# Kernel tuning notes

Measured on AMD Instinct MI355X. Metric: run time of the kernel, lower is better.

The kernel has to match this reference:

```python
import jax, jax.numpy as jnp
import numpy as np

N, D1, D2, B = 8, 2048, 1024, 512
D = D1 * D2
MAXBW = 3
NUM_PART = 5          # num_possible_partitions
TEMP = 0.01           # TEMPERATURE used in df_lt
DENOS = (3.0, 5.0, 17.0)  # 2^2-1, 2^2+1, 2^4+1


def ste_floor(x):
    # straight-through floor: forward floor, backward identity
    return x + jax.lax.stop_gradient(jnp.floor(x) - x)


def segmented_mean(piece, scheme, msp):
    """Replicates the inner python scan over sorted rows.
    piece:  (N, D) sorted residual errors
    scheme: (N-1, D) rounded split decisions (0/1), per column
    msp:    (N-1, D) soft split probabilities (grad factors), per column
    Returns (N, D): each row gets grad_ * (segment mean) of its segment.
    """
    n = piece.shape[0]
    buf = jnp.zeros_like(piece[0])
    cnt = jnp.zeros_like(piece[0])
    g = jnp.ones_like(piece[0])
    reset = jnp.zeros(piece.shape[1], dtype=bool)
    vlist, blist = [], []
    for i in range(n):
        buf = jnp.where(reset, piece[i], buf + piece[i])
        cnt = jnp.where(reset, 1.0, cnt + 1.0)
        g = jnp.where(reset, 1.0, g)
        if i == n - 1:
            vlist.append(g * (buf / cnt))
            blist.append(jnp.ones_like(reset))
        else:
            b = scheme[i] > 0.5
            vlist.append(jnp.where(b, g * msp[i], 0.0) * (buf / cnt))
            blist.append(b)
            g = jnp.where(b, g, g * (1.0 - msp[i]))
            reset = b
    # broadcast each segment-end value back to all rows of its segment
    out = vlist[-1]
    outs = [out]
    for i in range(n - 2, -1, -1):
        out = jnp.where(blist[i], vlist[i], out)
        outs.append(out)
    return jnp.stack(outs[::-1], axis=0)


def residual_quant(U, vsum, s, thr):
    """One residual quantization level (the update_partition=True branch)."""
    res = U - vsum                                   # (N, D)
    idx_maps = jnp.argsort(res, axis=0)              # torch.sort ascending, dim=0
    sorted_err = jnp.take_along_axis(res, idx_maps, axis=0)
    delta = sorted_err[1:] - sorted_err[:-1]         # (N-1, D), >= 0
    delta = delta / jnp.max(delta)
    msp = jax.nn.sigmoid((delta - thr) / TEMP)       # mean_split_point (N-1, D)
    rs = jnp.round(msp)                              # round_split, 0/1

    nm1 = N - 1
    P = 2 ** nm1  # all possible split-column patterns (torch.unique over dim=1)
    weights = (2 ** jnp.arange(nm1 - 1, -1, -1)).astype(jnp.int32)  # row 0 = MSB (lexicographic)
    code = jnp.sum(rs.astype(jnp.int32) * weights[:, None], axis=0)  # (D,)
    counts = jnp.zeros((P,), jnp.int32).at[code].add(1)
    present = counts > 0
    # torch.unique sorts patterns lexicographically -> rank = #present codes below
    rank_of_code = jnp.cumsum(present.astype(jnp.int32)) - present.astype(jnp.int32)
    order = jnp.argsort(-counts)                     # codes by count descending
    top_codes = order[:NUM_PART]
    top_ranks = rank_of_code[top_codes]              # s_indices[:NUM_PART]
    # binary patterns for every possible code
    patterns = ((jnp.arange(P)[:, None] >> jnp.arange(nm1 - 1, -1, -1)[None, :]) & 1).astype(jnp.float32)  # (P, N-1)
    inter = patterns @ patterns[top_codes].T         # (P, NUM_PART)
    sel = jnp.argmax(inter, axis=1)
    reassigned = top_ranks[sel]                      # (P,)
    is_top = jnp.any(rank_of_code[:, None] == top_ranks[None, :], axis=1)
    final_rank = jnp.where(is_top, rank_of_code, reassigned)  # (P,)
    c_rank = final_rank[code]                        # clustered_indices, (D,)

    # NOTE: original indexes round_split / mean_split_point columns BY the
    # unique-cluster index value s_idx (a quirk of the source); replicate it.
    scheme_used = rs[:, c_rank]                      # (N-1, D)
    msp_used = msp[:, c_rank]                        # (N-1, D)

    inner = segmented_mean(sorted_err, scheme_used, msp_used)  # (N, D)
    # einsum('cb,cba->ab', inner, one_hot(idx_maps)) == unsort along dim 0
    inv = jnp.argsort(idx_maps, axis=0)
    grouped = jnp.take_along_axis(inner, inv, axis=0)
    return s * ste_floor(grouped / s)


def setup_inputs():
    key = jax.random.key(0)
    k1, k2 = jax.random.split(key)
    x = jax.random.normal(k1, (B, N, D1), dtype=jnp.float32)
    # kaiming_normal_ on (N, D): std = sqrt(2 / fan_in), fan_in = D
    U = jax.random.normal(k2, (N, D), dtype=jnp.float32) * np.float32(np.sqrt(2.0 / D))
    thres_mean = jnp.full((D2,), -1.3, dtype=jnp.float32)
    return {"x": x, "U": U, "thres_mean": thres_mean}


def reference(x, U, thres_mean):
    beta = jnp.max(U)
    alpha = jnp.min(U)
    s = (beta - alpha) / DENOS[0]
    vsum = s * ste_floor(U / s)                      # base quantization level
    thr = jax.nn.sigmoid(jnp.repeat(thres_mean, D1))  # thres_mean.repeat_interleave(D1)
    for deno in DENOS[1:MAXBW]:
        s = s / deno
        vsum = vsum + residual_quant(U, vsum, s, thr)
    w = vsum.reshape(N, D1, D2)
    return jnp.einsum('bnd,ndl->bnl', x, w)
```

## Files before the change

kernel.cpp:

```cpp
#include <hip/hip_runtime.h>
#include <hip/hip_bf16.h>
#include <math.h>

#define NROW 8
#define DT   2097152
#define DD1  2048
#define DD2  1024
#define BATCH 512
#define NBLK 2048


#define SL_SMAX 0
#define SL_SMIN 2048
#define SL_G2   4096
#define SL_G3   6144

typedef __attribute__((ext_vector_type(8))) short short8;
typedef __attribute__((ext_vector_type(4))) float f32x4;

__device__ __forceinline__ unsigned fenc(float f){
  unsigned u = __float_as_uint(f);
  return (u & 0x80000000u) ? ~u : (u | 0x80000000u);
}
__device__ __forceinline__ float fdec(unsigned k){
  return (k & 0x80000000u) ? __uint_as_float(k ^ 0x80000000u) : __uint_as_float(~k);
}
__device__ __forceinline__ float sigmoid_ref(float z){
  #pragma clang fp contract(off)
  return 1.0f / (1.0f + expf(-z));
}
__device__ __forceinline__ unsigned short f2bf(float f){
  __hip_bfloat16 h = __float2bfloat16(f);
  return *reinterpret_cast<unsigned short*>(&h);
}
__device__ __forceinline__ float base1(float u, float s1, float inv_s1){
  #pragma clang fp contract(off)
  return s1 * floorf(u * inv_s1);
}
__device__ __forceinline__ void async16(const unsigned short* g, unsigned short* l){
  __builtin_amdgcn_global_load_lds((const __attribute__((address_space(1))) unsigned int*)g,
                                   (__attribute__((address_space(3))) unsigned int*)l, 16, 0, 0);
}

#define CSWAPV(a,b) { float _lo=fminf(a,b), _hi=fmaxf(a,b); a=_lo; b=_hi; }
__device__ __forceinline__ void sort8v(float v[8]){
  CSWAPV(v[0],v[1]) CSWAPV(v[2],v[3]) CSWAPV(v[4],v[5]) CSWAPV(v[6],v[7])
  CSWAPV(v[0],v[2]) CSWAPV(v[1],v[3]) CSWAPV(v[4],v[6]) CSWAPV(v[5],v[7])
  CSWAPV(v[1],v[2]) CSWAPV(v[5],v[6])
  CSWAPV(v[0],v[4]) CSWAPV(v[1],v[5]) CSWAPV(v[2],v[6]) CSWAPV(v[3],v[7])
  CSWAPV(v[2],v[4]) CSWAPV(v[3],v[5])
  CSWAPV(v[1],v[2]) CSWAPV(v[3],v[4]) CSWAPV(v[5],v[6])
}
__device__ __forceinline__ void cswapkv(float&av,int&ai,float&bv,int&bi){
  bool sw = (av > bv) || ((av == bv) && (ai > bi));
  float nav = sw ? bv : av; float nbv = sw ? av : bv;
  int   nai = sw ? bi : ai; int   nbi = sw ? ai : bi;
  av = nav; bv = nbv; ai = nai; bi = nbi;
}
#define CSWAPK(i,j) cswapkv(v[i],ix[i],v[j],ix[j]);
__device__ __forceinline__ void sort8kv(float v[8], int ix[8]){
  CSWAPK(0,1) CSWAPK(2,3) CSWAPK(4,5) CSWAPK(6,7)
  CSWAPK(0,2) CSWAPK(1,3) CSWAPK(4,6) CSWAPK(5,7)
  CSWAPK(1,2) CSWAPK(5,6)
  CSWAPK(0,4) CSWAPK(1,5) CSWAPK(2,6) CSWAPK(3,7)
  CSWAPK(2,4) CSWAPK(3,5)
  CSWAPK(1,2) CSWAPK(3,4) CSWAPK(5,6)
}

template<int BD>
__device__ __forceinline__ unsigned slots_max(const unsigned* s, unsigned* red, int t){
  unsigned v = 0u;
  for (int i = t; i < NBLK; i += BD) v = max(v, s[i]);
  red[t] = v; __syncthreads();
  for (int o = BD/2; o > 0; o >>= 1){ if (t < o) red[t] = max(red[t], red[t+o]); __syncthreads(); }
  unsigned r = red[0]; __syncthreads(); return r;
}
template<int BD>
__device__ __forceinline__ unsigned slots_min(const unsigned* s, unsigned* red, int t){
  unsigned v = 0xFFFFFFFFu;
  for (int i = t; i < NBLK; i += BD) v = min(v, s[i]);
  red[t] = v; __syncthreads();
  for (int o = BD/2; o > 0; o >>= 1){ if (t < o) red[t] = min(red[t], red[t+o]); __syncthreads(); }
  unsigned r = red[0]; __syncthreads(); return r;
}
template<int BD>
__device__ __forceinline__ float get_s1(const unsigned* slots, unsigned* red, int t){
  float beta  = fdec(slots_max<BD>(slots + SL_SMAX, red, t));
  float alpha = fdec(slots_min<BD>(slots + SL_SMIN, red, t));
  return (beta - alpha) / 3.0f;
}
__device__ __forceinline__ float vn2_of(float u, unsigned char mb, float s1, float inv_s1, float s2){
  #pragma clang fp contract(off)
  return base1(u, s1, inv_s1) + s2 * (float)((int)mb - 8);
}

__global__ __launch_bounds__(256) void k_mmxb(const float* __restrict__ U, const float* __restrict__ x,
                                              unsigned short* __restrict__ xb,
                                              unsigned* __restrict__ meta, unsigned* __restrict__ slots){
  __shared__ unsigned redA[256], redB[256];
  int t = threadIdx.x, b = blockIdx.x;
  int gid = b*256 + t;
  if (b == 0 && t < 128){ meta[4+t] = 0u; meta[132+t] = 0u; }
  const float4* x4 = (const float4*)x;
  #pragma unroll
  for (int i = 0; i < 4; ++i){
    int idx = gid + i*524288;
    float4 v = x4[idx];
    ushort4 o;
    o.x = f2bf(v.x); o.y = f2bf(v.y); o.z = f2bf(v.z); o.w = f2bf(v.w);
    *(ushort4*)(xb + (size_t)idx*4) = o;
  }
  const float4* U4 = (const float4*)U;
  float mx = -INFINITY, mn = INFINITY;
  #pragma unroll
  for (int i = 0; i < 8; ++i){
    float4 v = U4[gid + i*524288];
    mx = fmaxf(mx, fmaxf(fmaxf(v.x,v.y), fmaxf(v.z,v.w)));
    mn = fminf(mn, fminf(fminf(v.x,v.y), fminf(v.z,v.w)));
  }
  redA[t] = fenc(mx); redB[t] = fenc(mn);
  __syncthreads();
  for (int o = 128; o > 0; o >>= 1){
    if (t < o){ redA[t] = max(redA[t], redA[t+o]); redB[t] = min(redB[t], redB[t+o]); }
    __syncthreads();
  }
  if (t == 0){ slots[SL_SMAX + b] = redA[0]; slots[SL_SMIN + b] = redB[0]; }
}

__global__ __launch_bounds__(256) void k_passA2(const float* __restrict__ U,
                                                unsigned* __restrict__ slots){
  #pragma clang fp contract(off)
  __shared__ unsigned red[256];
  int t = threadIdx.x, b = blockIdx.x;
  float s1 = get_s1<256>(slots, red, t);
  float inv_s1 = 1.0f / s1;
  int d0 = (b*256 + t)*4;
  float4 u[8];
  #pragma unroll
  for (int i = 0; i < 8; ++i) u[i] = *(const float4*)(U + (size_t)i*DT + d0);
  unsigned dmax = 0u;
  #pragma unroll
  for (int c = 0; c < 4; ++c){
    float res[8];
    #pragma unroll
    for (int i = 0; i < 8; ++i){
      float uv = ((const float*)&u[i])[c];
      res[i] = uv - base1(uv, s1, inv_s1);
    }
    sort8v(res);
    float m = 0.0f;
    #pragma unroll
    for (int i = 0; i < 7; ++i) m = fmaxf(m, res[i+1] - res[i]);
    dmax = max(dmax, __float_as_uint(m));
  }
  red[t] = dmax;
  __syncthreads();
  for (int o = 128; o > 0; o >>= 1){
    if (t < o) red[t] = max(red[t], red[t+o]);
    __syncthreads();
  }
  if (t == 0) slots[SL_G2 + b] = red[0];
}

template<int LEVEL>
__global__ __launch_bounds__(256) void k_passB(const float* __restrict__ U,
                                               const unsigned char* __restrict__ mcode,
                                               const float* __restrict__ tm,
                                               unsigned char* __restrict__ code,
                                               unsigned* __restrict__ meta, unsigned* __restrict__ slots){
  #pragma clang fp contract(off)
  __shared__ unsigned red[256];
  __shared__ int hist[128];
  int t = threadIdx.x, b = blockIdx.x;
  if (t < 128) hist[t] = 0;
  float s1 = get_s1<256>(slots, red, t);
  float inv_s1 = 1.0f / s1;
  float s2 = s1 / 5.0f;
  float gmax = __uint_as_float(slots_max<256>(slots + ((LEVEL==2)?SL_G2:SL_G3), red, t));
  float inv_gmax = 1.0f / gmax;
  int d0 = (b*256 + t)*4;
  float4 u[8], bb[8];
  #pragma unroll
  for (int i = 0; i < 8; ++i){
    u[i] = *(const float4*)(U + (size_t)i*DT + d0);
    if (LEVEL == 2){
      bb[i].x = base1(u[i].x, s1, inv_s1); bb[i].y = base1(u[i].y, s1, inv_s1);
      bb[i].z = base1(u[i].z, s1, inv_s1); bb[i].w = base1(u[i].w, s1, inv_s1);
    } else {
      uchar4 m4 = *(const uchar4*)(mcode + (size_t)i*DT + d0);
      bb[i].x = vn2_of(u[i].x, m4.x, s1, inv_s1, s2);
      bb[i].y = vn2_of(u[i].y, m4.y, s1, inv_s1, s2);
      bb[i].z = vn2_of(u[i].z, m4.z, s1, inv_s1, s2);
      bb[i].w = vn2_of(u[i].w, m4.w, s1, inv_s1, s2);
    }
  }
  float thr = sigmoid_ref(tm[d0 >> 11]);
  uchar4 cods;
  unsigned char* cp = (unsigned char*)&cods;
  #pragma unroll
  for (int c = 0; c < 4; ++c){
    float res[8];
    #pragma unroll
    for (int i = 0; i < 8; ++i) res[i] = ((const float*)&u[i])[c] - ((const float*)&bb[i])[c];
    sort8v(res);
    int cd = 0;
    #pragma unroll
    for (int i = 0; i < 7; ++i){
      float dn = (res[i+1] - res[i]) * inv_gmax;
      cd = (cd << 1) | ((dn > thr) ? 1 : 0);
    }
    cp[c] = (unsigned char)cd;
    atomicAdd(&hist[cd], 1);
  }
  *(uchar4*)(code + d0) = cods;
  __syncthreads();
  if (t < 128){ int h = hist[t]; if (h) atomicAdd((int*)&meta[((LEVEL==2)?4:132) + t], h); }
}

template<int LEVEL>
__global__ void k_small(const float* __restrict__ U, const unsigned char* __restrict__ mcode,
                        const float* __restrict__ tm, unsigned* __restrict__ meta,
                        unsigned* __restrict__ slots){
  #pragma clang fp contract(off)
  __shared__ unsigned red[128];
  __shared__ int cs[128], rk[128], redk[128];
  __shared__ int top_code[5], top_rank[5];
  __shared__ int w0cnt;
  int c = threadIdx.x;
  float s1 = get_s1<128>(slots, red, c);
  float inv_s1 = 1.0f / s1;
  float s2 = s1 / 5.0f;
  float gmax = __uint_as_float(slots_max<128>(slots + ((LEVEL==2)?SL_G2:SL_G3), red, c));
  cs[c] = (int)meta[((LEVEL==2)?4:132) + c];
  bool present = cs[c] > 0;
  unsigned long long bm = __ballot(present);
  int lane = c & 63;
  int r = (int)__popcll(bm & ((1ull << lane) - 1ull));
  if (c == 63) w0cnt = (int)__popcll(bm);
  __syncthreads();
  if (c >= 64) r += w0cnt;
  rk[c] = r;
  __syncthreads();
  for (int k = 0; k < 5; ++k){
    redk[c] = (cs[c] << 7) | (127 - c);
    __syncthreads();
    for (int o = 64; o > 0; o >>= 1){
      if (c < o) redk[c] = max(redk[c], redk[c+o]);
      __syncthreads();
    }
    if (c == 0){
      int best = 127 - (redk[0] & 127);
      top_code[k] = best; top_rank[k] = rk[best];
      cs[best] = -1;
    }
    __syncthreads();
  }
  int besti = -1, sel = 0;
  #pragma unroll
  for (int j = 0; j < 5; ++j){
    int inter = __popc(c & top_code[j]);
    if (inter > besti){ besti = inter; sel = j; }
  }
  bool is_top = false;
  #pragma unroll
  for (int j = 0; j < 5; ++j) is_top = is_top || (rk[c] == top_rank[j]);
  ((int*)meta)[260 + c] = is_top ? rk[c] : top_rank[sel];
  float res[8];
  #pragma unroll
  for (int i = 0; i < 8; ++i){
    size_t off = (size_t)i*DT + c;
    float u = U[off];
    float bval = (LEVEL==2) ? base1(u, s1, inv_s1) : vn2_of(u, mcode[off], s1, inv_s1, s2);
    res[i] = u - bval;
  }
  sort8v(res);
  float thr = sigmoid_ref(tm[c >> 11]);
  unsigned bits = 0;
  float* msp_tab = (float*)(meta + 388);
  #pragma unroll
  for (int i = 0; i < 7; ++i){
    float dn  = (res[i+1] - res[i]) / gmax;
    float z   = (dn - thr) / 0.01f;
    float msp = sigmoid_ref(z);
    msp_tab[c*7 + i] = msp;
    bits |= ((unsigned)(int)rintf(msp)) << i;
  }
  meta[1284 + c] = bits;
}

template<int LEVEL>
__global__ __launch_bounds__(256) void k_passD(const float* __restrict__ U,
                                               unsigned char* __restrict__ mcode,
                                               unsigned short* __restrict__ vsumb,
                                               const unsigned char* __restrict__ code,
                                               unsigned* __restrict__ meta, unsigned* __restrict__ slots){
  #pragma clang fp contract(off)
  __shared__ float q_lds[32*256];
  __shared__ unsigned red[256];
  __shared__ int fr_s[128];
  __shared__ unsigned bits_s[128];
  __shared__ float msp_s[896];
  int t = threadIdx.x, b = blockIdx.x;
  float s1 = get_s1<256>(slots, red, t);
  float inv_s1 = 1.0f / s1;
  float s2 = s1 / 5.0f;
  float s  = (LEVEL == 2) ? s2 : (s2 / 17.0f);
  float inv_s = 1.0f / s;
  if (t < 128){ fr_s[t] = ((const int*)meta)[260+t]; bits_s[t] = meta[1284+t]; }
  for (int i = t; i < 896; i += 256) msp_s[i] = ((const float*)(meta+388))[i];
  __syncthreads();
  int d0 = (b*256 + t)*4;
  float4 u4[8], b4[8];
  #pragma unroll
  for (int i = 0; i < 8; ++i){
    u4[i] = *(const float4*)(U + (size_t)i*DT + d0);
    if (LEVEL == 2){
      b4[i].x = base1(u4[i].x, s1, inv_s1); b4[i].y = base1(u4[i].y, s1, inv_s1);
      b4[i].z = base1(u4[i].z, s1, inv_s1); b4[i].w = base1(u4[i].w, s1, inv_s1);
    } else {
      uchar4 m4 = *(const uchar4*)(mcode + (size_t)i*DT + d0);
      b4[i].x = vn2_of(u4[i].x, m4.x, s1, inv_s1, s2);
      b4[i].y = vn2_of(u4[i].y, m4.y, s1, inv_s1, s2);
      b4[i].z = vn2_of(u4[i].z, m4.z, s1, inv_s1, s2);
      b4[i].w = vn2_of(u4[i].w, m4.w, s1, inv_s1, s2);
    }
  }
  uchar4 cods = *(const uchar4*)(code + d0);
  const unsigned char* cp = (const unsigned char*)&cods;
  #pragma unroll
  for (int c = 0; c < 4; ++c){
    float v[8]; int ix[8];
    #pragma unroll
    for (int i = 0; i < 8; ++i){
      v[i] = ((const float*)&u4[i])[c] - ((const float*)&b4[i])[c];
      ix[i] = i;
    }
    sort8kv(v, ix);
    int cr = fr_s[cp[c]];
    unsigned sb = bits_s[cr];
    float vv[8]; bool bl[8];
    float buf = 0.0f, cnt = 0.0f, g = 1.0f; bool reset = false;
    #pragma unroll
    for (int i = 0; i < 8; ++i){
      buf = reset ? v[i] : (buf + v[i]);
      cnt = reset ? 1.0f : (cnt + 1.0f);
      g   = reset ? 1.0f : g;
      float m = buf * __builtin_amdgcn_rcpf(cnt);
      if (i == 7){ vv[7] = g * m; bl[7] = true; }
      else {
        float msp = msp_s[cr*7 + i];
        bool bv = ((sb >> i) & 1u) != 0u;
        vv[i] = bv ? ((g * msp) * m) : 0.0f;
        bl[i] = bv;
        g = bv ? g : (g * (1.0f - msp));
        reset = bv;
      }
    }
    float out = vv[7];
    float inner[8];
    inner[7] = out;
    for (int i = 6; i >= 0; --i){ if (bl[i]) out = vv[i]; inner[i] = out; }
    #pragma unroll
    for (int i = 0; i < 8; ++i){
      float mf = floorf(inner[i] * inv_s);
      q_lds[(ix[i]*4 + c)*256 + t] = mf;
    }
  }
  unsigned dmax = 0u;
  if (LEVEL == 2){
    uchar4 mout[8];
    #pragma unroll
    for (int c = 0; c < 4; ++c){
      float res3[8];
      #pragma unroll
      for (int rr = 0; rr < 8; ++rr){
        int mi = (int)q_lds[(rr*4 + c)*256 + t];
        mi = max(-8, min(7, mi));
        float q = s * (float)mi;
        float vn = ((const float*)&b4[rr])[c] + q;
        ((unsigned char*)&mout[rr])[c] = (unsigned char)(mi + 8);
        res3[rr] = ((const float*)&u4[rr])[c] - vn;
      }
      sort8v(res3);
      float m = 0.0f;
      #pragma unroll
      for (int i = 0; i < 7; ++i) m = fmaxf(m, res3[i+1] - res3[i]);
      dmax = max(dmax, __float_as_uint(m));
    }
    #pragma unroll
    for (int rr = 0; rr < 8; ++rr)
      *(uchar4*)(mcode + (size_t)rr*DT + d0) = mout[rr];
    __syncthreads();
    red[t] = dmax;
    __syncthreads();
    for (int o = 128; o > 0; o >>= 1){
      if (t < o) red[t] = max(red[t], red[t+o]);
      __syncthreads();
    }
    if (t == 0) slots[SL_G3 + b] = red[0];
  } else {
    #pragma unroll
    for (int rr = 0; rr < 8; ++rr){
      ushort4 o;
      #pragma unroll
      for (int c = 0; c < 4; ++c){
        float q = s * q_lds[(rr*4 + c)*256 + t];
        float vn = ((const float*)&b4[rr])[c] + q;
        ((unsigned short*)&o)[c] = f2bf(vn);
      }
      *(ushort4*)(vsumb + (size_t)rr*DT + d0) = o;
    }
  }
}

__global__ __launch_bounds__(256) void k_wt(const unsigned short* __restrict__ vsumb,
                                            unsigned short* __restrict__ wt){
  __shared__ unsigned short tile[64][68];
  int t = threadIdx.x;
  int c4 = t & 15, r0 = t >> 4;
  int n = blockIdx.z, k0 = blockIdx.y*64, l0 = blockIdx.x*64;
  const unsigned short* src = vsumb + (size_t)n*DT;
  #pragma unroll
  for (int i = 0; i < 4; ++i){
    int r = r0 + i*16;
    ushort4 v = *(const ushort4*)(src + (size_t)(k0+r)*DD2 + l0 + c4*4);
    *(ushort4*)&tile[r][c4*4] = v;
  }
  __syncthreads();
  unsigned short* dst = wt + (size_t)n*DT;
  #pragma unroll
  for (int i = 0; i < 4; ++i){
    int rl = r0 + i*16;
    ushort4 o;
    o.x = tile[c4*4+0][rl]; o.y = tile[c4*4+1][rl];
    o.z = tile[c4*4+2][rl]; o.w = tile[c4*4+3][rl];
    *(ushort4*)(dst + (size_t)(l0+rl)*DD1 + k0 + c4*4) = o;
  }
}

__global__ __launch_bounds__(256) void k_gemm(const unsigned short* __restrict__ xb,
                                              const unsigned short* __restrict__ wt,
                                              float* __restrict__ out){
  __shared__ __align__(16) unsigned short As[64*64];
  __shared__ __align__(16) unsigned short Bs[128*64];
  int t = threadIdx.x;
  int lane = t & 63, wv = t >> 6;
  int n  = blockIdx.z;
  int b0 = blockIdx.y * 64;
  int l0 = blockIdx.x * 128;
  int wm = (wv >> 1) * 32, wn = (wv & 1) * 64;
  int col = lane & 15, quad = lane >> 4;
  int arow = lane >> 3, aseg = lane & 7;
  const unsigned short* wtn = wt + (size_t)n*DT;
  f32x4 acc[2][4] = {};
  for (int k0 = 0; k0 < DD1; k0 += 64){
    #pragma unroll
    for (int i = 0; i < 2; ++i){
      int row = wv*16 + i*8 + arow;
      const unsigned short* g = xb + (((size_t)(b0+row)*NROW + n)*DD1 + k0 + aseg*8);
      async16(g, &As[(wv*16 + i*8)*64]);
    }
    #pragma unroll
    for (int i = 0; i < 4; ++i){
      int row = wv*32 + i*8 + arow;
      const unsigned short* g = wtn + ((size_t)(l0+row)*DD1 + k0 + aseg*8);
      async16(g, &Bs[(wv*32 + i*8)*64]);
    }
    __syncthreads();
    #pragma unroll
    for (int ks = 0; ks < 2; ++ks){
      int kq = ks*32 + quad*8;
      short8 af[2], bfr[4];
      #pragma unroll
      for (int mi = 0; mi < 2; ++mi) af[mi]  = *(const short8*)&As[(wm + mi*16 + col)*64 + kq];
      #pragma unroll
      for (int ni = 0; ni < 4; ++ni) bfr[ni] = *(const short8*)&Bs[(wn + ni*16 + col)*64 + kq];
      #pragma unroll
      for (int mi = 0; mi < 2; ++mi)
        #pragma unroll
        for (int ni = 0; ni < 4; ++ni)
          acc[mi][ni] = __builtin_amdgcn_mfma_f32_16x16x32_bf16(af[mi], bfr[ni], acc[mi][ni], 0, 0, 0);
    }
    __syncthreads();
  }
  #pragma unroll
  for (int mi = 0; mi < 2; ++mi)
    #pragma unroll
    for (int ni = 0; ni < 4; ++ni)
      #pragma unroll
      for (int r = 0; r < 4; ++r){
        int bb = b0 + wm + mi*16 + quad*4 + r;
        int l = l0 + wn + ni*16 + col;
        out[((size_t)bb*NROW + n)*DD2 + l] = acc[mi][ni][r];
      }
}

extern "C" void kernel_launch(void* const* d_in, const int* in_sizes, int n_in,
                              void* d_out, int out_size, void* d_ws, size_t ws_size,
                              hipStream_t stream){
  const float* x  = (const float*)d_in[0];
  const float* U  = (const float*)d_in[1];
  const float* tm = (const float*)d_in[2];
  float* out = (float*)d_out;
  unsigned char*  mcode = (unsigned char*)d_ws;
  unsigned short* vsumb = (unsigned short*)((unsigned char*)d_ws + 16777216);
  unsigned short* xb    = (unsigned short*)((unsigned char*)d_ws + 50331648);
  unsigned char*  code  = (unsigned char*)d_ws + 67108864;
  unsigned short* wt    = (unsigned short*)((unsigned char*)d_ws + 69206016);
  unsigned* meta  = (unsigned*)((unsigned char*)d_ws + 102760448);
  unsigned* slots = (unsigned*)((unsigned char*)d_ws + 102768640);
  (void)in_sizes; (void)n_in; (void)out_size; (void)ws_size;

  k_mmxb    <<<NBLK, 256, 0, stream>>>(U, x, xb, meta, slots);
  k_passA2  <<<NBLK, 256, 0, stream>>>(U, slots);
  k_passB<2><<<NBLK, 256, 0, stream>>>(U, mcode, tm, code, meta, slots);
  k_small<2><<<1,   128, 0, stream>>>(U, mcode, tm, meta, slots);
  k_passD<2><<<NBLK, 256, 0, stream>>>(U, mcode, vsumb, code, meta, slots);
  k_passB<3><<<NBLK, 256, 0, stream>>>(U, mcode, tm, code, meta, slots);
  k_small<3><<<1,   128, 0, stream>>>(U, mcode, tm, meta, slots);
  k_passD<3><<<NBLK, 256, 0, stream>>>(U, mcode, vsumb, code, meta, slots);
  k_wt  <<<dim3(DD2/64, DD1/64, NROW), 256, 0, stream>>>(vsumb, wt);
  k_gemm<<<dim3(DD2/128, BATCH/64, NROW), 256, 0, stream>>>(xb, wt, out);
}
```

Baseline: 399.2 us.

## Precompute global reductions in tiny finalize kernels; aggregate histogram atomics per wave

Before, every block of the big passes re-reduced the 2048 per-block max/min slots to get s1 and gmax. That cost several block-wide barrier reductions per block. Now small single-block k_fin kernels do each reduction once and write s1 and gmax to a fin buffer, which the passes just load. The histogram update in passB also changes: lanes with equal codes are grouped by ballot and one leader does the atomicAdd, which cuts shared-memory atomic contention. The price is three extra kernel launches and a serial ballot loop whose trip count grows with the number of distinct codes per wave.

```diff
diff --git a/kernel.cpp b/kernel.cpp
--- a/kernel.cpp
+++ b/kernel.cpp
@@ -36,6 +36,10 @@
 __device__ __forceinline__ float base1(float u, float s1, float inv_s1){
   #pragma clang fp contract(off)
   return s1 * floorf(u * inv_s1);
+}
+__device__ __forceinline__ float vn2_of(float u, unsigned char mb, float s1, float inv_s1, float s2){
+  #pragma clang fp contract(off)
+  return base1(u, s1, inv_s1) + s2 * (float)((int)mb - 8);
 }
 __device__ __forceinline__ void async16(const unsigned short* g, unsigned short* l){
   __builtin_amdgcn_global_load_lds((const __attribute__((address_space(1))) unsigned int*)g,
@@ -67,33 +71,6 @@
   CSWAPK(1,2) CSWAPK(3,4) CSWAPK(5,6)
 }
 
-template<int BD>
-__device__ __forceinline__ unsigned slots_max(const unsigned* s, unsigned* red, int t){
-  unsigned v = 0u;
-  for (int i = t; i < NBLK; i += BD) v = max(v, s[i]);
-  red[t] = v; __syncthreads();
-  for (int o = BD/2; o > 0; o >>= 1){ if (t < o) red[t] = max(red[t], red[t+o]); __syncthreads(); }
-  unsigned r = red[0]; __syncthreads(); return r;
-}
-template<int BD>
-__device__ __forceinline__ unsigned slots_min(const unsigned* s, unsigned* red, int t){
-  unsigned v = 0xFFFFFFFFu;
-  for (int i = t; i < NBLK; i += BD) v = min(v, s[i]);
-  red[t] = v; __syncthreads();
-  for (int o = BD/2; o > 0; o >>= 1){ if (t < o) red[t] = min(red[t], red[t+o]); __syncthreads(); }
-  unsigned r = red[0]; __syncthreads(); return r;
-}
-template<int BD>
-__device__ __forceinline__ float get_s1(const unsigned* slots, unsigned* red, int t){
-  float beta  = fdec(slots_max<BD>(slots + SL_SMAX, red, t));
-  float alpha = fdec(slots_min<BD>(slots + SL_SMIN, red, t));
-  return (beta - alpha) / 3.0f;
-}
-__device__ __forceinline__ float vn2_of(float u, unsigned char mb, float s1, float inv_s1, float s2){
-  #pragma clang fp contract(off)
-  return base1(u, s1, inv_s1) + s2 * (float)((int)mb - 8);
-}
-
 __global__ __launch_bounds__(256) void k_mmxb(const float* __restrict__ U, const float* __restrict__ x,
                                               unsigned short* __restrict__ xb,
                                               unsigned* __restrict__ meta, unsigned* __restrict__ slots){
@@ -127,12 +104,44 @@
   if (t == 0){ slots[SL_SMAX + b] = redA[0]; slots[SL_SMIN + b] = redB[0]; }
 }
 
+template<int MODE>
+__global__ void k_fin(const unsigned* __restrict__ slots, unsigned* __restrict__ fin){
+  __shared__ unsigned redA[256], redB[256];
+  int t = threadIdx.x;
+  if (MODE == 0){
+    unsigned vx = 0u, vn = 0xFFFFFFFFu;
+    for (int i = t; i < NBLK; i += 256){ vx = max(vx, slots[SL_SMAX+i]); vn = min(vn, slots[SL_SMIN+i]); }
+    redA[t] = vx; redB[t] = vn;
+    __syncthreads();
+    for (int o = 128; o > 0; o >>= 1){
+      if (t < o){ redA[t] = max(redA[t], redA[t+o]); redB[t] = min(redB[t], redB[t+o]); }
+      __syncthreads();
+    }
+    if (t == 0){
+      float s1 = (fdec(redA[0]) - fdec(redB[0])) / 3.0f;
+      fin[0] = __float_as_uint(s1);
+    }
+  } else {
+    const unsigned* s = slots + ((MODE==1) ? SL_G2 : SL_G3);
+    unsigned vx = 0u;
+    for (int i = t; i < NBLK; i += 256) vx = max(vx, s[i]);
+    redA[t] = vx;
+    __syncthreads();
+    for (int o = 128; o > 0; o >>= 1){
+      if (t < o) redA[t] = max(redA[t], redA[t+o]);
+      __syncthreads();
+    }
+    if (t == 0) fin[MODE] = redA[0];
+  }
+}
+
 __global__ __launch_bounds__(256) void k_passA2(const float* __restrict__ U,
+                                                const unsigned* __restrict__ fin,
                                                 unsigned* __restrict__ slots){
   #pragma clang fp contract(off)
   __shared__ unsigned red[256];
   int t = threadIdx.x, b = blockIdx.x;
-  float s1 = get_s1<256>(slots, red, t);
+  float s1 = __uint_as_float(fin[0]);
   float inv_s1 = 1.0f / s1;
   int d0 = (b*256 + t)*4;
   float4 u[8];
@@ -167,16 +176,17 @@
                                                const unsigned char* __restrict__ mcode,
                                                const float* __restrict__ tm,
                                                unsigned char* __restrict__ code,
-                                               unsigned* __restrict__ meta, unsigned* __restrict__ slots){
-  #pragma clang fp contract(off)
-  __shared__ unsigned red[256];
+                                               unsigned* __restrict__ meta,
+                                               const unsigned* __restrict__ fin){
+  #pragma clang fp contract(off)
   __shared__ int hist[128];
   int t = threadIdx.x, b = blockIdx.x;
+  int lane = t & 63;
   if (t < 128) hist[t] = 0;
-  float s1 = get_s1<256>(slots, red, t);
+  float s1 = __uint_as_float(fin[0]);
   float inv_s1 = 1.0f / s1;
   float s2 = s1 / 5.0f;
-  float gmax = __uint_as_float(slots_max<256>(slots + ((LEVEL==2)?SL_G2:SL_G3), red, t));
+  float gmax = __uint_as_float(fin[(LEVEL==2)?1:2]);
   float inv_gmax = 1.0f / gmax;
   int d0 = (b*256 + t)*4;
   float4 u[8], bb[8];
@@ -194,6 +204,7 @@
       bb[i].w = vn2_of(u[i].w, m4.w, s1, inv_s1, s2);
     }
   }
+  __syncthreads();
   float thr = sigmoid_ref(tm[d0 >> 11]);
   uchar4 cods;
   unsigned char* cp = (unsigned char*)&cods;
@@ -210,7 +221,17 @@
       cd = (cd << 1) | ((dn > thr) ? 1 : 0);
     }
     cp[c] = (unsigned char)cd;
-    atomicAdd(&hist[cd], 1);
+    bool pending = true;
+    while (true){
+      unsigned long long nd = __ballot(pending);
+      if (nd == 0ull) break;
+      int leader = (int)__ffsll((unsigned long long)nd) - 1;
+      int lc = __shfl(cd, leader);
+      bool mine = pending && (cd == lc);
+      unsigned long long mm = __ballot(mine);
+      if (lane == leader) atomicAdd(&hist[lc], (int)__popcll(mm));
+      if (mine) pending = false;
+    }
   }
   *(uchar4*)(code + d0) = cods;
   __syncthreads();
@@ -220,17 +241,16 @@
 template<int LEVEL>
 __global__ void k_small(const float* __restrict__ U, const unsigned char* __restrict__ mcode,
                         const float* __restrict__ tm, unsigned* __restrict__ meta,
-                        unsigned* __restrict__ slots){
-  #pragma clang fp contract(off)
-  __shared__ unsigned red[128];
+                        const unsigned* __restrict__ fin){
+  #pragma clang fp contract(off)
   __shared__ int cs[128], rk[128], redk[128];
   __shared__ int top_code[5], top_rank[5];
   __shared__ int w0cnt;
   int c = threadIdx.x;
-  float s1 = get_s1<128>(slots, red, c);
+  float s1 = __uint_as_float(fin[0]);
   float inv_s1 = 1.0f / s1;
   float s2 = s1 / 5.0f;
-  float gmax = __uint_as_float(slots_max<128>(slots + ((LEVEL==2)?SL_G2:SL_G3), red, c));
+  float gmax = __uint_as_float(fin[(LEVEL==2)?1:2]);
   cs[c] = (int)meta[((LEVEL==2)?4:132) + c];
   bool present = cs[c] > 0;
   unsigned long long bm = __ballot(present);
@@ -293,7 +313,9 @@
                                                unsigned char* __restrict__ mcode,
                                                unsigned short* __restrict__ vsumb,
                                                const unsigned char* __restrict__ code,
-                                               unsigned* __restrict__ meta, unsigned* __restrict__ slots){
+                                               unsigned* __restrict__ meta,
+                                               const unsigned* __restrict__ fin,
+                                               unsigned* __restrict__ slots){
   #pragma clang fp contract(off)
   __shared__ float q_lds[32*256];
   __shared__ unsigned red[256];
@@ -301,7 +323,7 @@
   __shared__ unsigned bits_s[128];
   __shared__ float msp_s[896];
   int t = threadIdx.x, b = blockIdx.x;
-  float s1 = get_s1<256>(slots, red, t);
+  float s1 = __uint_as_float(fin[0]);
   float inv_s1 = 1.0f / s1;
   float s2 = s1 / 5.0f;
   float s  = (LEVEL == 2) ? s2 : (s2 / 17.0f);
@@ -509,16 +531,20 @@
   unsigned short* wt    = (unsigned short*)((unsigned char*)d_ws + 69206016);
   unsigned* meta  = (unsigned*)((unsigned char*)d_ws + 102760448);
   unsigned* slots = (unsigned*)((unsigned char*)d_ws + 102768640);
+  unsigned* fin   = (unsigned*)((unsigned char*)d_ws + 102801408);
   (void)in_sizes; (void)n_in; (void)out_size; (void)ws_size;
 
   k_mmxb    <<<NBLK, 256, 0, stream>>>(U, x, xb, meta, slots);
-  k_passA2  <<<NBLK, 256, 0, stream>>>(U, slots);
-  k_passB<2><<<NBLK, 256, 0, stream>>>(U, mcode, tm, code, meta, slots);
-  k_small<2><<<1,   128, 0, stream>>>(U, mcode, tm, meta, slots);
-  k_passD<2><<<NBLK, 256, 0, stream>>>(U, mcode, vsumb, code, meta, slots);
-  k_passB<3><<<NBLK, 256, 0, stream>>>(U, mcode, tm, code, meta, slots);
-  k_small<3><<<1,   128, 0, stream>>>(U, mcode, tm, meta, slots);
-  k_passD<3><<<NBLK, 256, 0, stream>>>(U, mcode, vsumb, code, meta, slots);
+  k_fin<0>  <<<1,    256, 0, stream>>>(slots, fin);
+  k_passA2  <<<NBLK, 256, 0, stream>>>(U, fin, slots);
+  k_fin<1>  <<<1,    256, 0, stream>>>(slots, fin);
+  k_passB<2><<<NBLK, 256, 0, stream>>>(U, mcode, tm, code, meta, fin);
+  k_small<2><<<1,   128, 0, stream>>>(U, mcode, tm, meta, fin);
+  k_passD<2><<<NBLK, 256, 0, stream>>>(U, mcode, vsumb, code, meta, fin, slots);
+  k_fin<2>  <<<1,    256, 0, stream>>>(slots, fin);
+  k_passB<3><<<NBLK, 256, 0, stream>>>(U, mcode, tm, code, meta, fin);
+  k_small<3><<<1,   128, 0, stream>>>(U, mcode, tm, meta, fin);
+  k_passD<3><<<NBLK, 256, 0, stream>>>(U, mcode, vsumb, code, meta, fin, slots);
   k_wt  <<<dim3(DD2/64, DD1/64, NROW), 256, 0, stream>>>(vsumb, wt);
   k_gemm<<<dim3(DD2/128, BATCH/64, NROW), 256, 0, stream>>>(xb, wt, out);
 }
```

Result: faster. 386.2 us (-3.3%).
